# Kernel tuning notes

Hardware: AMD Instinct MI355X
Metric: run time of the kernel (lower is better)

## Reference

```python
import jax, jax.numpy as jnp
import numpy as np

N = 50000      # nodes
E = 1250000    # edges (avg degree 32)
D = 64         # in_channels == hidden_channels
L = 3          # num_layers
IMPROVED_FILL = 2.0  # GCNConv(improved=True) self-loop weight


def setup_inputs() -> dict:
    key = jax.random.key(0)
    ks = jax.random.split(key, 6)
    x = jax.random.normal(ks[0], (N, D), dtype=jnp.float32)
    edge_index = jax.random.randint(ks[1], (2, E), 0, N, dtype=jnp.int64)
    edge_weight = jax.random.uniform(ks[2], (E,), dtype=jnp.float32)
    Ws = jax.random.normal(ks[3], (L, D, D), dtype=jnp.float32) / np.sqrt(D).astype(np.float32)
    bs = jnp.zeros((L, D), dtype=jnp.float32)
    Wf = jax.random.normal(ks[4], (D, 1), dtype=jnp.float32) / np.sqrt(D).astype(np.float32)
    bf = jnp.zeros((1,), dtype=jnp.float32)
    return dict(x=x, edge_index=edge_index, edge_weight=edge_weight,
                Ws=Ws, bs=bs, Wf=Wf, bf=bf, prob=0)


def _gcn_norm(edge_index, edge_weight, n):
    # add self-loops with fill value 2.0 (improved=True)
    loop = jnp.arange(n, dtype=edge_index.dtype)
    row = jnp.concatenate([edge_index[0], loop])  # source nodes (x_j)
    col = jnp.concatenate([edge_index[1], loop])  # target nodes (aggregation)
    w = jnp.concatenate([edge_weight,
                         jnp.full((n,), IMPROVED_FILL, edge_weight.dtype)])
    deg = jax.ops.segment_sum(w, col, num_segments=n)
    dis = jnp.where(deg > 0, jax.lax.rsqrt(deg), 0.0)  # deg^{-1/2}, inf->0
    norm = dis[row] * w * dis[col]                      # [E+N]
    return row, col, norm


def reference(x, edge_index, edge_weight, Ws, bs, Wf, bf, prob):
    n = x.shape[0]
    # gcn_norm depends only on graph structure; compute once, reuse per layer
    row, col, norm = _gcn_norm(edge_index, edge_weight, n)
    for l in range(Ws.shape[0]):
        h = x @ Ws[l]                                  # [N, D] linear transform
        msg = h[row] * norm[:, None]                   # gather + per-edge scale
        agg = jax.ops.segment_sum(msg, col, num_segments=n)  # scatter-add
        x = jax.nn.relu(agg + bs[l])
    # F.dropout(x, p=prob) with prob=0 -> identity (inference)
    return x @ Wf + bf                                 # [N, 1]
```

## Files before the change

### kernel.cpp

```cpp
#include <hip/hip_runtime.h>
#include <hip/hip_bf16.h>

#define DCH 64
#define NB_CSR 256
#define MAXBINS 256

typedef __attribute__((ext_vector_type(8))) short bfrag;
typedef __attribute__((ext_vector_type(4))) float ffrag;

static __device__ __forceinline__ unsigned short f2bf(float f) {
    unsigned u = __float_as_uint(f);
    unsigned r = (u + 0x7fffu + ((u >> 16) & 1u)) >> 16;
    return (unsigned short)r;
}
static __device__ __forceinline__ float bf2f(unsigned short s) {
    return __uint_as_float(((unsigned)s) << 16);
}

__global__ __launch_bounds__(1024) void binc_k(const int* __restrict__ col,
                                               unsigned* __restrict__ blkcnt, int e) {
    __shared__ unsigned bins[MAXBINS];
    int B = blockIdx.x, tid = threadIdx.x;
    int chunk = (e + NB_CSR - 1) / NB_CSR;
    int beg = B * chunk, end = min(e, beg + chunk);
    if (tid < MAXBINS) bins[tid] = 0;
    __syncthreads();
    for (int i = beg + tid; i < end; i += 1024)
        atomicAdd(&bins[col[i] >> 8], 1u);
    __syncthreads();
    if (tid < MAXBINS) blkcnt[B * MAXBINS + tid] = bins[tid];
}

__global__ __launch_bounds__(256) void bincur_k(const unsigned* __restrict__ blkcnt,
                                                unsigned* __restrict__ blkcur,
                                                int* __restrict__ binbase,
                                                int* __restrict__ ptr,
                                                int nbins, int n, int e) {
    __shared__ unsigned tot[MAXBINS];
    __shared__ unsigned base[MAXBINS + 1];
    int j = threadIdx.x;
    unsigned t = 0;
    if (j < nbins) {
        for (int B = 0; B < NB_CSR; B += 8) {
            t += blkcnt[(B + 0) * MAXBINS + j] + blkcnt[(B + 1) * MAXBINS + j]
               + blkcnt[(B + 2) * MAXBINS + j] + blkcnt[(B + 3) * MAXBINS + j]
               + blkcnt[(B + 4) * MAXBINS + j] + blkcnt[(B + 5) * MAXBINS + j]
               + blkcnt[(B + 6) * MAXBINS + j] + blkcnt[(B + 7) * MAXBINS + j];
        }
    }
    tot[j] = t;
    __syncthreads();
    if (j == 0) {
        unsigned run = 0;
        for (int k = 0; k < nbins; ++k) { base[k] = run; run += tot[k]; }
        base[nbins] = run;
    }
    __syncthreads();
    if (j < nbins) {
        unsigned run = base[j];
        binbase[j] = (int)run;
        for (int B = 0; B < NB_CSR; B += 4) {
            unsigned c0 = blkcnt[(B + 0) * MAXBINS + j];
            unsigned c1 = blkcnt[(B + 1) * MAXBINS + j];
            unsigned c2 = blkcnt[(B + 2) * MAXBINS + j];
            unsigned c3 = blkcnt[(B + 3) * MAXBINS + j];
            blkcur[(B + 0) * MAXBINS + j] = run;  run += c0;
            blkcur[(B + 1) * MAXBINS + j] = run;  run += c1;
            blkcur[(B + 2) * MAXBINS + j] = run;  run += c2;
            blkcur[(B + 3) * MAXBINS + j] = run;  run += c3;
        }
    }
    if (j == 0) { binbase[nbins] = e; ptr[n] = e; }
}

__global__ __launch_bounds__(1024) void binfill_k(const int* __restrict__ row,
                                                  const int* __restrict__ col,
                                                  const float* __restrict__ ew,
                                                  const unsigned* __restrict__ blkcur,
                                                  uint2* __restrict__ rec, int e) {
    __shared__ unsigned cur[MAXBINS];
    int B = blockIdx.x, tid = threadIdx.x;
    int chunk = (e + NB_CSR - 1) / NB_CSR;
    int beg = B * chunk, end = min(e, beg + chunk);
    if (tid < MAXBINS) cur[tid] = blkcur[B * MAXBINS + tid];
    __syncthreads();
    for (int i = beg + tid; i < end; i += 1024) {
        int c = col[i];
        unsigned slot = atomicAdd(&cur[c >> 8], 1u);
        rec[slot] = make_uint2((unsigned)row[i] | ((unsigned)(c & 255) << 20),
                               __float_as_uint(ew[i]));
    }
}

__global__ __launch_bounds__(1024) void csr_k(const uint2* __restrict__ rec,
                                              const int* __restrict__ binbase,
                                              int* __restrict__ ptr,
                                              uint2* __restrict__ edg,
                                              float* __restrict__ dis, int n) {
    __shared__ unsigned ncnt[256];
    __shared__ unsigned nbase[256];
    __shared__ float degs[256];
    int b = blockIdx.x, tid = threadIdx.x;
    int beg = binbase[b], end = binbase[b + 1];
    int node0 = b << 8;
    int nn = min(256, n - node0);
    if (tid < 256) { ncnt[tid] = 0; degs[tid] = 0.f; }
    __syncthreads();
    for (int i = beg + tid; i < end; i += 1024) {
        uint2 r = rec[i];
        unsigned c8 = r.x >> 20;
        atomicAdd(&ncnt[c8], 1u);
        atomicAdd(&degs[c8], __uint_as_float(r.y));
    }
    __syncthreads();
    if (tid == 0) {
        unsigned run = (unsigned)beg;
        for (int k = 0; k < 256; ++k) { nbase[k] = run; run += ncnt[k]; }
    }
    __syncthreads();
    if (tid < nn) {
        ptr[node0 + tid] = (int)nbase[tid];
        dis[node0 + tid] = rsqrtf(degs[tid] + 2.0f);
    }
    if (tid < 256) ncnt[tid] = 0;
    __syncthreads();
    for (int i = beg + tid; i < end; i += 1024) {
        uint2 r = rec[i];
        unsigned c8 = r.x >> 20;
        unsigned pos = nbase[c8] + atomicAdd(&ncnt[c8], 1u);
        edg[pos] = make_uint2(r.x & 0xFFFFFu, r.y);
    }
}

__global__ __launch_bounds__(256) void normw_k(uint2* __restrict__ edg,
                                               const float* __restrict__ dis, int e) {
    int i = blockIdx.x * 256 + threadIdx.x;
    if (i >= e) return;
    uint2 ev = edg[i];
    ((unsigned*)edg)[2 * i + 1] =
        __float_as_uint(__uint_as_float(ev.y) * dis[ev.x]);
}

__global__ __launch_bounds__(256) void pack_k(const float* __restrict__ Ws,
                                              short* __restrict__ wpk, int L) {
    int ent = blockIdx.x * 256 + threadIdx.x;
    if (ent >= L * 512) return;
    int layer = ent >> 9;
    int r = ent & 511;
    int lane = r & 63;
    int st = r >> 6;
    int s = st >> 2, t = st & 3;
    int quad = lane >> 4;
    int ncol = t * 16 + (lane & 15);
    const float* W = Ws + (size_t)layer * DCH * DCH;
    union { short sh[8]; int4 v; } hi, lo;
#pragma unroll
    for (int j = 0; j < 8; ++j) {
        int k = s * 32 + quad * 8 + j;
        float w = W[k * DCH + ncol];
        unsigned short h = f2bf(w);
        hi.sh[j] = (short)h;
        lo.sh[j] = (short)f2bf(w - bf2f(h));
    }
    *(int4*)(wpk + ((size_t)(layer * 2 + 0) * 512 + r) * 8) = hi.v;
    *(int4*)(wpk + ((size_t)(layer * 2 + 1) * 512 + r) * 8) = lo.v;
}

__global__ __launch_bounds__(256) void gemm_k(const float* __restrict__ x,
                                              const short* __restrict__ wpk_layer,
                                              unsigned short* __restrict__ hb, int n_tiles) {
    __shared__ short Wl[2][512 * 8];
    {
        const int4* src = (const int4*)wpk_layer;
        int4* dst = (int4*)&Wl[0][0];
        for (int i = threadIdx.x; i < 1024; i += 256) dst[i] = src[i];
    }
    __syncthreads();
    int wave = threadIdx.x >> 6, lane = threadIdx.x & 63;
    int tile = blockIdx.x * 4 + wave;
    if (tile >= n_tiles) return;
    int m = lane & 15, quad = lane >> 4;
    int row = tile * 16 + m;

    float av[2][8];
    {
        const float4* p0 = (const float4*)(x + (size_t)row * DCH + quad * 8);
        const float4* p1 = (const float4*)(x + (size_t)row * DCH + 32 + quad * 8);
        float4 a0 = p0[0], a1 = p0[1], b0 = p1[0], b1 = p1[1];
        av[0][0] = a0.x; av[0][1] = a0.y; av[0][2] = a0.z; av[0][3] = a0.w;
        av[0][4] = a1.x; av[0][5] = a1.y; av[0][6] = a1.z; av[0][7] = a1.w;
        av[1][0] = b0.x; av[1][1] = b0.y; av[1][2] = b0.z; av[1][3] = b0.w;
        av[1][4] = b1.x; av[1][5] = b1.y; av[1][6] = b1.z; av[1][7] = b1.w;
    }
    bfrag ah[2], al[2];
#pragma unroll
    for (int s = 0; s < 2; ++s)
#pragma unroll
        for (int j = 0; j < 8; ++j) {
            unsigned short hbv = f2bf(av[s][j]);
            ah[s][j] = (short)hbv;
            al[s][j] = (short)f2bf(av[s][j] - bf2f(hbv));
        }

#pragma unroll
    for (int t = 0; t < 4; ++t) {
        ffrag acc = {0.f, 0.f, 0.f, 0.f};
#pragma unroll
        for (int s = 0; s < 2; ++s) {
            bfrag wh = *(bfrag*)&Wl[0][((s * 4 + t) * 64 + lane) * 8];
            bfrag wl = *(bfrag*)&Wl[1][((s * 4 + t) * 64 + lane) * 8];
            acc = __builtin_amdgcn_mfma_f32_16x16x32_bf16(ah[s], wh, acc, 0, 0, 0);
            acc = __builtin_amdgcn_mfma_f32_16x16x32_bf16(al[s], wh, acc, 0, 0, 0);
            acc = __builtin_amdgcn_mfma_f32_16x16x32_bf16(ah[s], wl, acc, 0, 0, 0);
        }
        int colc = t * 16 + m;
#pragma unroll
        for (int r = 0; r < 4; ++r)
            hb[(size_t)(tile * 16 + quad * 4 + r) * DCH + colc] = f2bf(acc[r]);
    }
}

static __device__ __forceinline__ void gather_node(int node, int lane, int p, int hf,
                                                   float dis_c,
                                                   const int* __restrict__ ptr,
                                                   const uint2* __restrict__ edg,
                                                   const unsigned* __restrict__ hbf,
                                                   float& A0, float& A1) {
    float a0 = 0.f, a1 = 0.f;
    if (hf == 0) {
        unsigned sv = hbf[(size_t)node * 32 + p];
        a0 = 2.0f * dis_c * __uint_as_float(sv << 16);
        a1 = 2.0f * dis_c * __uint_as_float(sv & 0xffff0000u);
    }
    int beg = ptr[node], end = ptr[node + 1];
    for (int base = beg; base < end; base += 64) {
        int idx = base + lane;
        int rv = 0; float nv = 0.f;
        if (idx < end) {
            uint2 ev = edg[idx];
            rv = (int)ev.x;
            nv = __uint_as_float(ev.y);
        }
        int m = min(64, end - base);
        int steps = (((m + 1) >> 1) + 7) & ~7;
        for (int j0 = 0; j0 < steps; j0 += 8) {
            unsigned hv[8]; float nn[8];
#pragma unroll
            for (int q = 0; q < 8; ++q) {
                int eidx = 2 * (j0 + q) + hf;
                int r = __shfl(rv, eidx);
                nn[q] = __shfl(nv, eidx);
                hv[q] = hbf[(size_t)r * 32 + p];
            }
#pragma unroll
            for (int q = 0; q < 8; ++q) {
                a0 += __uint_as_float(hv[q] << 16) * nn[q];
                a1 += __uint_as_float(hv[q] & 0xffff0000u) * nn[q];
            }
        }
    }
    A0 = a0 + __shfl_xor(a0, 32);
    A1 = a1 + __shfl_xor(a1, 32);
}

__global__ __launch_bounds__(256) void gg_k(const int* __restrict__ ptr,
                                            const uint2* __restrict__ edg,
                                            const float* __restrict__ dis,
                                            const unsigned* __restrict__ hbf,
                                            const float* __restrict__ b,
                                            const short* __restrict__ wpk_next,
                                            unsigned short* __restrict__ hb_out, int n) {
    __shared__ float xs[16][68];
    int w = threadIdx.x >> 6, lane = threadIdx.x & 63;
    int p = lane & 31, hf = lane >> 5;
    int tile = blockIdx.x;
    float2 bv = ((const float2*)b)[p];
#pragma unroll 1
    for (int i = 0; i < 4; ++i) {
        int node = tile * 16 + w * 4 + i;
        if (node < n) {
            float dis_c = dis[node];
            float A0, A1;
            gather_node(node, lane, p, hf, dis_c, ptr, edg, hbf, A0, A1);
            if (hf == 0) {
                xs[w * 4 + i][2 * p]     = fmaxf(dis_c * A0 + bv.x, 0.f);
                xs[w * 4 + i][2 * p + 1] = fmaxf(dis_c * A1 + bv.y, 0.f);
            }
        }
    }
    __syncthreads();
    int m = lane & 15, quad = lane >> 4, t = w;
    bfrag ah[2], al[2];
#pragma unroll
    for (int s = 0; s < 2; ++s)
#pragma unroll
        for (int j = 0; j < 8; ++j) {
            float v = xs[m][s * 32 + quad * 8 + j];
            unsigned short hbv = f2bf(v);
            ah[s][j] = (short)hbv;
            al[s][j] = (short)f2bf(v - bf2f(hbv));
        }
    ffrag acc = {0.f, 0.f, 0.f, 0.f};
#pragma unroll
    for (int s = 0; s < 2; ++s) {
        bfrag wh = *(const bfrag*)(wpk_next + ((size_t)((s * 4 + t) * 64 + lane)) * 8);
        bfrag wl = *(const bfrag*)(wpk_next + ((size_t)(512 + (s * 4 + t) * 64 + lane)) * 8);
        acc = __builtin_amdgcn_mfma_f32_16x16x32_bf16(ah[s], wh, acc, 0, 0, 0);
        acc = __builtin_amdgcn_mfma_f32_16x16x32_bf16(al[s], wh, acc, 0, 0, 0);
        acc = __builtin_amdgcn_mfma_f32_16x16x32_bf16(ah[s], wl, acc, 0, 0, 0);
    }
    int colc = t * 16 + m;
#pragma unroll
    for (int r = 0; r < 4; ++r) {
        int orow = tile * 16 + quad * 4 + r;
        if (orow < n) hb_out[(size_t)orow * DCH + colc] = f2bf(acc[r]);
    }
}

__global__ __launch_bounds__(256) void gf_k(const int* __restrict__ ptr,
                                            const uint2* __restrict__ edg,
                                            const float* __restrict__ dis,
                                            const unsigned* __restrict__ hbf,
                                            const float* __restrict__ b,
                                            const float* __restrict__ Wf,
                                            const float* __restrict__ bf,
                                            float* __restrict__ out, int n) {
    int node = blockIdx.x * 4 + (threadIdx.x >> 6);
    int lane = threadIdx.x & 63;
    if (node >= n) return;
    int p = lane & 31, hf = lane >> 5;
    float dis_c = dis[node];
    float A0, A1;
    gather_node(node, lane, p, hf, dis_c, ptr, edg, hbf, A0, A1);
    float2 bv = ((const float2*)b)[p];
    float2 wv = ((const float2*)Wf)[p];
    float x0 = fmaxf(dis_c * A0 + bv.x, 0.f);
    float x1 = fmaxf(dis_c * A1 + bv.y, 0.f);
    float v = x0 * wv.x + x1 * wv.y;
#pragma unroll
    for (int off = 16; off > 0; off >>= 1) v += __shfl_down(v, off);
    if (lane == 0) out[node] = v + bf[0];
}

extern "C" void kernel_launch(void* const* d_in, const int* in_sizes, int n_in,
                              void* d_out, int out_size, void* d_ws, size_t ws_size,
                              hipStream_t stream) {
    const float* x0 = (const float*)d_in[0];
    const int*   ei = (const int*)d_in[1];
    const float* ew = (const float*)d_in[2];
    const float* Ws = (const float*)d_in[3];
    const float* bs = (const float*)d_in[4];
    const float* Wf = (const float*)d_in[5];
    const float* bf = (const float*)d_in[6];

    const int n = in_sizes[0] / DCH;
    const int e = in_sizes[2];
    const int L = in_sizes[3] / (DCH * DCH);

    const int* row = ei;
    const int* col = ei + e;
    const int nbins = (n + 255) >> 8;

    size_t off = 0;
    auto alloc = [&](size_t bytes) {
        off = (off + 255) & ~(size_t)255;
        void* r = (char*)d_ws + off;
        off += bytes;
        return r;
    };
    int*      ptr     = (int*)     alloc((size_t)(n + 1) * 4);
    float*    dis     = (float*)   alloc((size_t)n * 4);
    short*    wpk     = (short*)   alloc((size_t)L * 2 * 512 * 8 * 2);
    uint2*    edg     = (uint2*)   alloc((size_t)e * 8);
    unsigned* blkcnt  = (unsigned*)alloc((size_t)NB_CSR * MAXBINS * 4);
    unsigned* blkcur  = (unsigned*)alloc((size_t)NB_CSR * MAXBINS * 4);
    int*      binbase = (int*)     alloc((size_t)(MAXBINS + 1) * 4);
    size_t szR = (size_t)e * 8;
    size_t szH = (size_t)2 * n * DCH * 2;
    unsigned char* regA = (unsigned char*)alloc(szR > szH ? szR : szH);
    uint2* rec = (uint2*)regA;
    unsigned short* hb_a = (unsigned short*)regA;
    unsigned short* hb_b = hb_a + (size_t)n * DCH;

    dim3 blk(256);
    const int n_tiles = (n + 15) / 16;

    binc_k   <<<dim3(NB_CSR), dim3(1024), 0, stream>>>(col, blkcnt, e);
    bincur_k <<<dim3(1), blk, 0, stream>>>(blkcnt, blkcur, binbase, ptr, nbins, n, e);
    binfill_k<<<dim3(NB_CSR), dim3(1024), 0, stream>>>(row, col, ew, blkcur, rec, e);
    csr_k    <<<dim3(nbins), dim3(1024), 0, stream>>>(rec, binbase, ptr, edg, dis, n);
    normw_k  <<<dim3((e + 255) / 256), blk, 0, stream>>>(edg, dis, e);
    pack_k   <<<dim3((L * 512 + 255) / 256), blk, 0, stream>>>(Ws, wpk, L);

    const size_t wstride = (size_t)2 * 512 * 8;
    gemm_k<<<dim3((n_tiles + 3) / 4), blk, 0, stream>>>(x0, wpk, hb_a, n_tiles);
    gg_k  <<<dim3(n_tiles), blk, 0, stream>>>(ptr, edg, dis, (const unsigned*)hb_a,
                                              bs, wpk + wstride, hb_b, n);
    gg_k  <<<dim3(n_tiles), blk, 0, stream>>>(ptr, edg, dis, (const unsigned*)hb_b,
                                              bs + DCH, wpk + 2 * wstride, hb_a, n);
    gf_k  <<<dim3((n + 3) / 4), blk, 0, stream>>>(ptr, edg, dis, (const unsigned*)hb_a,
                                                  bs + 2 * DCH, Wf, bf, (float*)d_out, n);
}
```

Baseline: 223.0 us.

## Split features into channel-half planes and unfuse gather from next-layer GEMM

Node features are stored as two 32-channel planes, and the aggregation kernel runs with a 2-D grid so each block gathers only one half. The smaller per-plane footprint is meant to improve cache locality for random neighbour gathers. Each wave now processes four edges in parallel with 16 lanes per edge, and edge records are read with nontemporal loads. The fused gather+GEMM kernels are split into a gather kernel that writes hi/lo bf16 activations and a separate MFMA GEMM kernel. The final projection now sums partials in an extra kernel, and weight packing is folded into the scan kernel, at the cost of extra launches and intermediate traffic.

```diff
diff --git a/kernel.cpp b/kernel.cpp
--- a/kernel.cpp
+++ b/kernel.cpp
@@ -35,7 +35,33 @@
                                                 unsigned* __restrict__ blkcur,
                                                 int* __restrict__ binbase,
                                                 int* __restrict__ ptr,
-                                                int nbins, int n, int e) {
+                                                int nbins, int n, int e,
+                                                const float* __restrict__ Ws,
+                                                short* __restrict__ wpk, int L) {
+    if (blockIdx.x == 1) {
+        for (int ent = threadIdx.x; ent < L * 512; ent += 256) {
+            int layer = ent >> 9;
+            int r = ent & 511;
+            int lane = r & 63;
+            int st = r >> 6;
+            int s = st >> 2, t = st & 3;
+            int quad = lane >> 4;
+            int ncol = t * 16 + (lane & 15);
+            const float* W = Ws + (size_t)layer * DCH * DCH;
+            union { short sh[8]; int4 v; } hi, lo;
+#pragma unroll
+            for (int j = 0; j < 8; ++j) {
+                int k = s * 32 + quad * 8 + j;
+                float w = W[k * DCH + ncol];
+                unsigned short h = f2bf(w);
+                hi.sh[j] = (short)h;
+                lo.sh[j] = (short)f2bf(w - bf2f(h));
+            }
+            *(int4*)(wpk + ((size_t)(layer * 2 + 0) * 512 + r) * 8) = hi.v;
+            *(int4*)(wpk + ((size_t)(layer * 2 + 1) * 512 + r) * 8) = lo.v;
+        }
+        return;
+    }
     __shared__ unsigned tot[MAXBINS];
     __shared__ unsigned base[MAXBINS + 1];
     int j = threadIdx.x;
@@ -141,34 +167,10 @@
         __float_as_uint(__uint_as_float(ev.y) * dis[ev.x]);
 }
 
-__global__ __launch_bounds__(256) void pack_k(const float* __restrict__ Ws,
-                                              short* __restrict__ wpk, int L) {
-    int ent = blockIdx.x * 256 + threadIdx.x;
-    if (ent >= L * 512) return;
-    int layer = ent >> 9;
-    int r = ent & 511;
-    int lane = r & 63;
-    int st = r >> 6;
-    int s = st >> 2, t = st & 3;
-    int quad = lane >> 4;
-    int ncol = t * 16 + (lane & 15);
-    const float* W = Ws + (size_t)layer * DCH * DCH;
-    union { short sh[8]; int4 v; } hi, lo;
-#pragma unroll
-    for (int j = 0; j < 8; ++j) {
-        int k = s * 32 + quad * 8 + j;
-        float w = W[k * DCH + ncol];
-        unsigned short h = f2bf(w);
-        hi.sh[j] = (short)h;
-        lo.sh[j] = (short)f2bf(w - bf2f(h));
-    }
-    *(int4*)(wpk + ((size_t)(layer * 2 + 0) * 512 + r) * 8) = hi.v;
-    *(int4*)(wpk + ((size_t)(layer * 2 + 1) * 512 + r) * 8) = lo.v;
-}
-
-__global__ __launch_bounds__(256) void gemm_k(const float* __restrict__ x,
-                                              const short* __restrict__ wpk_layer,
-                                              unsigned short* __restrict__ hb, int n_tiles) {
+__global__ __launch_bounds__(256) void gemm0_k(const float* __restrict__ x,
+                                               const short* __restrict__ wpk_layer,
+                                               unsigned short* __restrict__ hb,
+                                               int n, int n_tiles) {
     __shared__ short Wl[2][512 * 8];
     {
         const int4* src = (const int4*)wpk_layer;
@@ -181,6 +183,7 @@
     if (tile >= n_tiles) return;
     int m = lane & 15, quad = lane >> 4;
     int row = tile * 16 + m;
+    size_t nstride = (size_t)n * 32;
 
     float av[2][8];
     {
@@ -214,132 +217,144 @@
             acc = __builtin_amdgcn_mfma_f32_16x16x32_bf16(ah[s], wl, acc, 0, 0, 0);
         }
         int colc = t * 16 + m;
+        int pl = colc >> 5, c31 = colc & 31;
 #pragma unroll
         for (int r = 0; r < 4; ++r)
-            hb[(size_t)(tile * 16 + quad * 4 + r) * DCH + colc] = f2bf(acc[r]);
-    }
-}
-
-static __device__ __forceinline__ void gather_node(int node, int lane, int p, int hf,
-                                                   float dis_c,
-                                                   const int* __restrict__ ptr,
-                                                   const uint2* __restrict__ edg,
-                                                   const unsigned* __restrict__ hbf,
-                                                   float& A0, float& A1) {
-    float a0 = 0.f, a1 = 0.f;
-    if (hf == 0) {
-        unsigned sv = hbf[(size_t)node * 32 + p];
-        a0 = 2.0f * dis_c * __uint_as_float(sv << 16);
-        a1 = 2.0f * dis_c * __uint_as_float(sv & 0xffff0000u);
-    }
-    int beg = ptr[node], end = ptr[node + 1];
-    for (int base = beg; base < end; base += 64) {
-        int idx = base + lane;
-        int rv = 0; float nv = 0.f;
-        if (idx < end) {
-            uint2 ev = edg[idx];
-            rv = (int)ev.x;
-            nv = __uint_as_float(ev.y);
-        }
-        int m = min(64, end - base);
-        int steps = (((m + 1) >> 1) + 7) & ~7;
-        for (int j0 = 0; j0 < steps; j0 += 8) {
-            unsigned hv[8]; float nn[8];
-#pragma unroll
-            for (int q = 0; q < 8; ++q) {
-                int eidx = 2 * (j0 + q) + hf;
-                int r = __shfl(rv, eidx);
-                nn[q] = __shfl(nv, eidx);
-                hv[q] = hbf[(size_t)r * 32 + p];
-            }
-#pragma unroll
-            for (int q = 0; q < 8; ++q) {
-                a0 += __uint_as_float(hv[q] << 16) * nn[q];
-                a1 += __uint_as_float(hv[q] & 0xffff0000u) * nn[q];
-            }
-        }
-    }
-    A0 = a0 + __shfl_xor(a0, 32);
-    A1 = a1 + __shfl_xor(a1, 32);
-}
-
-__global__ __launch_bounds__(256) void gg_k(const int* __restrict__ ptr,
+            hb[pl * nstride + (size_t)(tile * 16 + quad * 4 + r) * 32 + c31] = f2bf(acc[r]);
+    }
+}
+
+__global__ __launch_bounds__(256) void gh_k(const int* __restrict__ ptr,
                                             const uint2* __restrict__ edg,
                                             const float* __restrict__ dis,
-                                            const unsigned* __restrict__ hbf,
+                                            const unsigned short* __restrict__ hplane,
                                             const float* __restrict__ b,
-                                            const short* __restrict__ wpk_next,
-                                            unsigned short* __restrict__ hb_out, int n) {
-    __shared__ float xs[16][68];
+                                            const float* __restrict__ Wf,
+                                            unsigned short* __restrict__ xhi,
+                                            unsigned short* __restrict__ xlo,
+                                            float* __restrict__ partial,
+                                            int n, int mode) {
+    int s = blockIdx.y;
+    size_t nstride = (size_t)n * 32;
+    const unsigned short* hp = hplane + s * nstride;
     int w = threadIdx.x >> 6, lane = threadIdx.x & 63;
-    int p = lane & 31, hf = lane >> 5;
-    int tile = blockIdx.x;
-    float2 bv = ((const float2*)b)[p];
+    int p16 = lane & 15, grp = lane >> 4;
+    int nd0 = blockIdx.x * 16 + w * 4;
+    if (nd0 >= n) return;
+    int bg[4], en[4]; float dc[4];
+#pragma unroll
+    for (int i = 0; i < 4; ++i) {
+        int nd = min(nd0 + i, n - 1);
+        bg[i] = ptr[nd]; en[i] = ptr[nd + 1]; dc[i] = dis[nd];
+    }
+    const unsigned long long* e8 = (const unsigned long long*)edg;
+    float2 bv = ((const float2*)b)[s * 16 + p16];
+    float2 wv = ((const float2*)Wf)[s * 16 + p16];
 #pragma unroll 1
     for (int i = 0; i < 4; ++i) {
-        int node = tile * 16 + w * 4 + i;
-        if (node < n) {
-            float dis_c = dis[node];
-            float A0, A1;
-            gather_node(node, lane, p, hf, dis_c, ptr, edg, hbf, A0, A1);
-            if (hf == 0) {
-                xs[w * 4 + i][2 * p]     = fmaxf(dis_c * A0 + bv.x, 0.f);
-                xs[w * 4 + i][2 * p + 1] = fmaxf(dis_c * A1 + bv.y, 0.f);
+        int node = nd0 + i;
+        if (node >= n) break;
+        float dis_c = dc[i];
+        float a0 = 0.f, a1 = 0.f;
+        if (grp == 0) {
+            unsigned sv = *(const unsigned*)(hp + (size_t)node * 32 + 2 * p16);
+            a0 = 2.0f * dis_c * __uint_as_float(sv << 16);
+            a1 = 2.0f * dis_c * __uint_as_float(sv & 0xffff0000u);
+        }
+        for (int base = bg[i]; base < en[i]; base += 64) {
+            int idx = base + lane;
+            unsigned long long ev = (idx < en[i])
+                ? __builtin_nontemporal_load(e8 + idx) : 0ull;
+            int rv = (int)(unsigned)ev;
+            float nv = __uint_as_float((unsigned)(ev >> 32));
+            int m = min(64, en[i] - base);
+            int ns8 = (((m + 3) >> 2) + 7) & ~7;
+            for (int j0 = 0; j0 < ns8; j0 += 8) {
+                unsigned hv[8]; float nn[8];
+#pragma unroll
+                for (int q = 0; q < 8; ++q) {
+                    int eidx = (j0 + q) * 4 + grp;
+                    int r = __shfl(rv, eidx);
+                    nn[q] = __shfl(nv, eidx);
+                    hv[q] = *(const unsigned*)(hp + (size_t)r * 32 + 2 * p16);
+                }
+#pragma unroll
+                for (int q = 0; q < 8; ++q) {
+                    a0 += __uint_as_float(hv[q] << 16) * nn[q];
+                    a1 += __uint_as_float(hv[q] & 0xffff0000u) * nn[q];
+                }
             }
         }
-    }
-    __syncthreads();
-    int m = lane & 15, quad = lane >> 4, t = w;
+        a0 += __shfl_xor(a0, 16); a0 += __shfl_xor(a0, 32);
+        a1 += __shfl_xor(a1, 16); a1 += __shfl_xor(a1, 32);
+        float x0 = fmaxf(dis_c * a0 + bv.x, 0.f);
+        float x1 = fmaxf(dis_c * a1 + bv.y, 0.f);
+        if (mode == 0) {
+            if (grp == 0) {
+                unsigned short h0 = f2bf(x0), h1 = f2bf(x1);
+                unsigned short l0 = f2bf(x0 - bf2f(h0)), l1 = f2bf(x1 - bf2f(h1));
+                *(unsigned*)(xhi + s * nstride + (size_t)node * 32 + 2 * p16) =
+                    (unsigned)h0 | ((unsigned)h1 << 16);
+                *(unsigned*)(xlo + s * nstride + (size_t)node * 32 + 2 * p16) =
+                    (unsigned)l0 | ((unsigned)l1 << 16);
+            }
+        } else {
+            float v = x0 * wv.x + x1 * wv.y;
+            v += __shfl_down(v, 8); v += __shfl_down(v, 4);
+            v += __shfl_down(v, 2); v += __shfl_down(v, 1);
+            if (lane == 0) partial[2 * node + s] = v;
+        }
+    }
+}
+
+__global__ __launch_bounds__(256) void gemmn_k(const unsigned short* __restrict__ xhi,
+                                               const unsigned short* __restrict__ xlo,
+                                               const short* __restrict__ wpk_layer,
+                                               unsigned short* __restrict__ hb,
+                                               int n, int n_tiles) {
+    __shared__ short Wl[2][512 * 8];
+    {
+        const int4* src = (const int4*)wpk_layer;
+        int4* dst = (int4*)&Wl[0][0];
+        for (int i = threadIdx.x; i < 1024; i += 256) dst[i] = src[i];
+    }
+    __syncthreads();
+    int wave = threadIdx.x >> 6, lane = threadIdx.x & 63;
+    int tile = blockIdx.x * 4 + wave;
+    if (tile >= n_tiles) return;
+    int m = lane & 15, quad = lane >> 4;
+    int row = tile * 16 + m;
+    size_t nstride = (size_t)n * 32;
     bfrag ah[2], al[2];
 #pragma unroll
-    for (int s = 0; s < 2; ++s)
-#pragma unroll
-        for (int j = 0; j < 8; ++j) {
-            float v = xs[m][s * 32 + quad * 8 + j];
-            unsigned short hbv = f2bf(v);
-            ah[s][j] = (short)hbv;
-            al[s][j] = (short)f2bf(v - bf2f(hbv));
-        }
-    ffrag acc = {0.f, 0.f, 0.f, 0.f};
-#pragma unroll
     for (int s = 0; s < 2; ++s) {
-        bfrag wh = *(const bfrag*)(wpk_next + ((size_t)((s * 4 + t) * 64 + lane)) * 8);
-        bfrag wl = *(const bfrag*)(wpk_next + ((size_t)(512 + (s * 4 + t) * 64 + lane)) * 8);
-        acc = __builtin_amdgcn_mfma_f32_16x16x32_bf16(ah[s], wh, acc, 0, 0, 0);
-        acc = __builtin_amdgcn_mfma_f32_16x16x32_bf16(al[s], wh, acc, 0, 0, 0);
-        acc = __builtin_amdgcn_mfma_f32_16x16x32_bf16(ah[s], wl, acc, 0, 0, 0);
-    }
-    int colc = t * 16 + m;
-#pragma unroll
-    for (int r = 0; r < 4; ++r) {
-        int orow = tile * 16 + quad * 4 + r;
-        if (orow < n) hb_out[(size_t)orow * DCH + colc] = f2bf(acc[r]);
-    }
-}
-
-__global__ __launch_bounds__(256) void gf_k(const int* __restrict__ ptr,
-                                            const uint2* __restrict__ edg,
-                                            const float* __restrict__ dis,
-                                            const unsigned* __restrict__ hbf,
-                                            const float* __restrict__ b,
-                                            const float* __restrict__ Wf,
-                                            const float* __restrict__ bf,
-                                            float* __restrict__ out, int n) {
-    int node = blockIdx.x * 4 + (threadIdx.x >> 6);
-    int lane = threadIdx.x & 63;
-    if (node >= n) return;
-    int p = lane & 31, hf = lane >> 5;
-    float dis_c = dis[node];
-    float A0, A1;
-    gather_node(node, lane, p, hf, dis_c, ptr, edg, hbf, A0, A1);
-    float2 bv = ((const float2*)b)[p];
-    float2 wv = ((const float2*)Wf)[p];
-    float x0 = fmaxf(dis_c * A0 + bv.x, 0.f);
-    float x1 = fmaxf(dis_c * A1 + bv.y, 0.f);
-    float v = x0 * wv.x + x1 * wv.y;
-#pragma unroll
-    for (int off = 16; off > 0; off >>= 1) v += __shfl_down(v, off);
-    if (lane == 0) out[node] = v + bf[0];
+        ah[s] = *(const bfrag*)(xhi + s * nstride + (size_t)row * 32 + quad * 8);
+        al[s] = *(const bfrag*)(xlo + s * nstride + (size_t)row * 32 + quad * 8);
+    }
+#pragma unroll
+    for (int t = 0; t < 4; ++t) {
+        ffrag acc = {0.f, 0.f, 0.f, 0.f};
+#pragma unroll
+        for (int s = 0; s < 2; ++s) {
+            bfrag wh = *(bfrag*)&Wl[0][((s * 4 + t) * 64 + lane) * 8];
+            bfrag wl = *(bfrag*)&Wl[1][((s * 4 + t) * 64 + lane) * 8];
+            acc = __builtin_amdgcn_mfma_f32_16x16x32_bf16(ah[s], wh, acc, 0, 0, 0);
+            acc = __builtin_amdgcn_mfma_f32_16x16x32_bf16(al[s], wh, acc, 0, 0, 0);
+            acc = __builtin_amdgcn_mfma_f32_16x16x32_bf16(ah[s], wl, acc, 0, 0, 0);
+        }
+        int colc = t * 16 + m;
+        int pl = colc >> 5, c31 = colc & 31;
+#pragma unroll
+        for (int r = 0; r < 4; ++r)
+            hb[pl * nstride + (size_t)(tile * 16 + quad * 4 + r) * 32 + c31] = f2bf(acc[r]);
+    }
+}
+
+__global__ __launch_bounds__(256) void fsum_k(const float* __restrict__ partial,
+                                              const float* __restrict__ bf,
+                                              float* __restrict__ out, int n) {
+    int i = blockIdx.x * 256 + threadIdx.x;
+    if (i < n) out[i] = partial[2 * i] + partial[2 * i + 1] + bf[0];
 }
 
 extern "C" void kernel_launch(void* const* d_in, const int* in_sizes, int n_in,
@@ -368,36 +383,41 @@
         off += bytes;
         return r;
     };
+    const size_t nstride = (size_t)n * 32;
     int*      ptr     = (int*)     alloc((size_t)(n + 1) * 4);
     float*    dis     = (float*)   alloc((size_t)n * 4);
+    float*    partial = (float*)   alloc((size_t)n * 2 * 4);
     short*    wpk     = (short*)   alloc((size_t)L * 2 * 512 * 8 * 2);
     uint2*    edg     = (uint2*)   alloc((size_t)e * 8);
     unsigned* blkcnt  = (unsigned*)alloc((size_t)NB_CSR * MAXBINS * 4);
     unsigned* blkcur  = (unsigned*)alloc((size_t)NB_CSR * MAXBINS * 4);
     int*      binbase = (int*)     alloc((size_t)(MAXBINS + 1) * 4);
-    size_t szR = (size_t)e * 8;
-    size_t szH = (size_t)2 * n * DCH * 2;
-    unsigned char* regA = (unsigned char*)alloc(szR > szH ? szR : szH);
+    size_t szR = (size_t)e * 8, szX = 4 * nstride * 2;
+    unsigned char* regA = (unsigned char*)alloc(szR > szX ? szR : szX);
     uint2* rec = (uint2*)regA;
-    unsigned short* hb_a = (unsigned short*)regA;
-    unsigned short* hb_b = hb_a + (size_t)n * DCH;
+    unsigned short* xhi = (unsigned short*)regA;
+    unsigned short* xlo = xhi + 2 * nstride;
+    unsigned short* hb  = (unsigned short*)alloc(2 * nstride * 2);
 
     dim3 blk(256);
     const int n_tiles = (n + 15) / 16;
+    const dim3 gh_grid((n + 15) / 16, 2);
 
     binc_k   <<<dim3(NB_CSR), dim3(1024), 0, stream>>>(col, blkcnt, e);
-    bincur_k <<<dim3(1), blk, 0, stream>>>(blkcnt, blkcur, binbase, ptr, nbins, n, e);
+    bincur_k <<<dim3(2), blk, 0, stream>>>(blkcnt, blkcur, binbase, ptr, nbins, n, e, Ws, wpk, L);
     binfill_k<<<dim3(NB_CSR), dim3(1024), 0, stream>>>(row, col, ew, blkcur, rec, e);
     csr_k    <<<dim3(nbins), dim3(1024), 0, stream>>>(rec, binbase, ptr, edg, dis, n);
     normw_k  <<<dim3((e + 255) / 256), blk, 0, stream>>>(edg, dis, e);
-    pack_k   <<<dim3((L * 512 + 255) / 256), blk, 0, stream>>>(Ws, wpk, L);
 
     const size_t wstride = (size_t)2 * 512 * 8;
-    gemm_k<<<dim3((n_tiles + 3) / 4), blk, 0, stream>>>(x0, wpk, hb_a, n_tiles);
-    gg_k  <<<dim3(n_tiles), blk, 0, stream>>>(ptr, edg, dis, (const unsigned*)hb_a,
-                                              bs, wpk + wstride, hb_b, n);
-    gg_k  <<<dim3(n_tiles), blk, 0, stream>>>(ptr, edg, dis, (const unsigned*)hb_b,
-                                              bs + DCH, wpk + 2 * wstride, hb_a, n);
-    gf_k  <<<dim3((n + 3) / 4), blk, 0, stream>>>(ptr, edg, dis, (const unsigned*)hb_a,
-                                                  bs + 2 * DCH, Wf, bf, (float*)d_out, n);
-}
+    gemm0_k<<<dim3((n_tiles + 3) / 4), blk, 0, stream>>>(x0, wpk, hb, n, n_tiles);
+    gh_k   <<<gh_grid, blk, 0, stream>>>(ptr, edg, dis, hb, bs, Wf,
+                                         xhi, xlo, partial, n, 0);
+    gemmn_k<<<dim3((n_tiles + 3) / 4), blk, 0, stream>>>(xhi, xlo, wpk + wstride, hb, n, n_tiles);
+    gh_k   <<<gh_grid, blk, 0, stream>>>(ptr, edg, dis, hb, bs + DCH, Wf,
+                                         xhi, xlo, partial, n, 0);
+    gemmn_k<<<dim3((n_tiles + 3) / 4), blk, 0, stream>>>(xhi, xlo, wpk + 2 * wstride, hb, n, n_tiles);
+    gh_k   <<<gh_grid, blk, 0, stream>>>(ptr, edg, dis, hb, bs + 2 * DCH, Wf,
+                                         xhi, xlo, partial, n, 1);
+    fsum_k <<<dim3((n + 255) / 256), blk, 0, stream>>>(partial, bf, (float*)d_out, n);
+}
```

New measurement: 283.4 us. +27.1%, slower.

## Parallelize bin offset scan across blocks and widen gather unroll to 16

Applied to the files above, without the earlier changes.

The single-block bincur kernel, which serially walks 256 blocks per bin and has one thread do the bin prefix, is split in two. One kernel runs a wavefront-level scan per bin across blocks. A second kernel scans the bin totals and writes the bin bases, which binfill now adds on the fly. Separately, the edge gather loop in the aggregation helper is unrolled to 16 loads in flight instead of 8. This raises memory-level parallelism at the cost of more registers and more padded steps for low-degree nodes.

```diff
diff --git a/kernel.cpp b/kernel.cpp
--- a/kernel.cpp
+++ b/kernel.cpp
@@ -31,58 +31,64 @@
     if (tid < MAXBINS) blkcnt[B * MAXBINS + tid] = bins[tid];
 }
 
-__global__ __launch_bounds__(256) void bincur_k(const unsigned* __restrict__ blkcnt,
+__global__ __launch_bounds__(64) void bincur1_k(const unsigned* __restrict__ blkcnt,
                                                 unsigned* __restrict__ blkcur,
-                                                int* __restrict__ binbase,
-                                                int* __restrict__ ptr,
-                                                int nbins, int n, int e) {
-    __shared__ unsigned tot[MAXBINS];
-    __shared__ unsigned base[MAXBINS + 1];
-    int j = threadIdx.x;
-    unsigned t = 0;
-    if (j < nbins) {
-        for (int B = 0; B < NB_CSR; B += 8) {
-            t += blkcnt[(B + 0) * MAXBINS + j] + blkcnt[(B + 1) * MAXBINS + j]
-               + blkcnt[(B + 2) * MAXBINS + j] + blkcnt[(B + 3) * MAXBINS + j]
-               + blkcnt[(B + 4) * MAXBINS + j] + blkcnt[(B + 5) * MAXBINS + j]
-               + blkcnt[(B + 6) * MAXBINS + j] + blkcnt[(B + 7) * MAXBINS + j];
-        }
-    }
-    tot[j] = t;
-    __syncthreads();
-    if (j == 0) {
-        unsigned run = 0;
-        for (int k = 0; k < nbins; ++k) { base[k] = run; run += tot[k]; }
-        base[nbins] = run;
-    }
-    __syncthreads();
-    if (j < nbins) {
-        unsigned run = base[j];
-        binbase[j] = (int)run;
-        for (int B = 0; B < NB_CSR; B += 4) {
-            unsigned c0 = blkcnt[(B + 0) * MAXBINS + j];
-            unsigned c1 = blkcnt[(B + 1) * MAXBINS + j];
-            unsigned c2 = blkcnt[(B + 2) * MAXBINS + j];
-            unsigned c3 = blkcnt[(B + 3) * MAXBINS + j];
-            blkcur[(B + 0) * MAXBINS + j] = run;  run += c0;
-            blkcur[(B + 1) * MAXBINS + j] = run;  run += c1;
-            blkcur[(B + 2) * MAXBINS + j] = run;  run += c2;
-            blkcur[(B + 3) * MAXBINS + j] = run;  run += c3;
-        }
-    }
-    if (j == 0) { binbase[nbins] = e; ptr[n] = e; }
+                                                unsigned* __restrict__ tot) {
+    int j = blockIdx.x, lane = threadIdx.x;
+    unsigned carry = 0;
+#pragma unroll
+    for (int c = 0; c < NB_CSR; c += 64) {
+        unsigned v = blkcnt[(size_t)(c + lane) * MAXBINS + j];
+        unsigned s = v;
+#pragma unroll
+        for (int off = 1; off < 64; off <<= 1) {
+            unsigned t = __shfl_up(s, off);
+            if (lane >= off) s += t;
+        }
+        blkcur[(size_t)(c + lane) * MAXBINS + j] = carry + s - v;
+        carry += __shfl(s, 63);
+    }
+    if (lane == 0) tot[j] = carry;
+}
+
+__global__ __launch_bounds__(256) void bincur2_k(const unsigned* __restrict__ tot,
+                                                 int* __restrict__ binbase,
+                                                 int* __restrict__ ptr,
+                                                 int nbins, int n, int e) {
+    __shared__ int wtot[4];
+    int tid = threadIdx.x, lane = tid & 63, w = tid >> 6;
+    int v = (tid < nbins) ? (int)tot[tid] : 0;
+    int s = v;
+#pragma unroll
+    for (int off = 1; off < 64; off <<= 1) {
+        int t = __shfl_up(s, off);
+        if (lane >= off) s += t;
+    }
+    if (lane == 63) wtot[w] = s;
+    __syncthreads();
+    if (tid == 0) {
+        int r = 0;
+#pragma unroll
+        for (int k = 0; k < 4; ++k) { int t = wtot[k]; wtot[k] = r; r += t; }
+    }
+    __syncthreads();
+    int excl = s - v + wtot[w];
+    if (tid < nbins) binbase[tid] = excl;
+    if (tid == 0) { binbase[nbins] = e; ptr[n] = e; }
 }
 
 __global__ __launch_bounds__(1024) void binfill_k(const int* __restrict__ row,
                                                   const int* __restrict__ col,
                                                   const float* __restrict__ ew,
                                                   const unsigned* __restrict__ blkcur,
+                                                  const int* __restrict__ binbase,
                                                   uint2* __restrict__ rec, int e) {
     __shared__ unsigned cur[MAXBINS];
     int B = blockIdx.x, tid = threadIdx.x;
     int chunk = (e + NB_CSR - 1) / NB_CSR;
     int beg = B * chunk, end = min(e, beg + chunk);
-    if (tid < MAXBINS) cur[tid] = blkcur[B * MAXBINS + tid];
+    if (tid < MAXBINS) cur[tid] = blkcur[(size_t)B * MAXBINS + tid]
+                                + (unsigned)binbase[tid];
     __syncthreads();
     for (int i = beg + tid; i < end; i += 1024) {
         int c = col[i];
@@ -242,18 +248,18 @@
             nv = __uint_as_float(ev.y);
         }
         int m = min(64, end - base);
-        int steps = (((m + 1) >> 1) + 7) & ~7;
-        for (int j0 = 0; j0 < steps; j0 += 8) {
-            unsigned hv[8]; float nn[8];
-#pragma unroll
-            for (int q = 0; q < 8; ++q) {
+        int steps = (((m + 1) >> 1) + 15) & ~15;
+        for (int j0 = 0; j0 < steps; j0 += 16) {
+            unsigned hv[16]; float nn[16];
+#pragma unroll
+            for (int q = 0; q < 16; ++q) {
                 int eidx = 2 * (j0 + q) + hf;
                 int r = __shfl(rv, eidx);
                 nn[q] = __shfl(nv, eidx);
                 hv[q] = hbf[(size_t)r * 32 + p];
             }
 #pragma unroll
-            for (int q = 0; q < 8; ++q) {
+            for (int q = 0; q < 16; ++q) {
                 a0 += __uint_as_float(hv[q] << 16) * nn[q];
                 a1 += __uint_as_float(hv[q] & 0xffff0000u) * nn[q];
             }
@@ -374,6 +380,7 @@
     uint2*    edg     = (uint2*)   alloc((size_t)e * 8);
     unsigned* blkcnt  = (unsigned*)alloc((size_t)NB_CSR * MAXBINS * 4);
     unsigned* blkcur  = (unsigned*)alloc((size_t)NB_CSR * MAXBINS * 4);
+    unsigned* tot     = (unsigned*)alloc((size_t)MAXBINS * 4);
     int*      binbase = (int*)     alloc((size_t)(MAXBINS + 1) * 4);
     size_t szR = (size_t)e * 8;
     size_t szH = (size_t)2 * n * DCH * 2;
@@ -386,8 +393,9 @@
     const int n_tiles = (n + 15) / 16;
 
     binc_k   <<<dim3(NB_CSR), dim3(1024), 0, stream>>>(col, blkcnt, e);
-    bincur_k <<<dim3(1), blk, 0, stream>>>(blkcnt, blkcur, binbase, ptr, nbins, n, e);
-    binfill_k<<<dim3(NB_CSR), dim3(1024), 0, stream>>>(row, col, ew, blkcur, rec, e);
+    bincur1_k<<<dim3(nbins), dim3(64), 0, stream>>>(blkcnt, blkcur, tot);
+    bincur2_k<<<dim3(1), blk, 0, stream>>>(tot, binbase, ptr, nbins, n, e);
+    binfill_k<<<dim3(NB_CSR), dim3(1024), 0, stream>>>(row, col, ew, blkcur, binbase, rec, e);
     csr_k    <<<dim3(nbins), dim3(1024), 0, stream>>>(rec, binbase, ptr, edg, dis, n);
     normw_k  <<<dim3((e + 255) / 256), blk, 0, stream>>>(edg, dis, e);
     pack_k   <<<dim3((L * 512 + 255) / 256), blk, 0, stream>>>(Ws, wpk, L);
```

New measurement: 220.8 us. Within noise of the previous version (-1.0%).
